# Optimization experiments

Measured on AMD Instinct MI355X. Metric: run time of the kernel, lower is better.

Reference implementation:

```python
import jax, jax.numpy as jnp
import numpy as np

B, N = 2, 512
CS, CZ, C, H, PQK, PV = 256, 128, 128, 8, 8, 12
INF, EPS = 1e5, 1e-8
ROPE_BASE = 10000.0


def _rotate_half(x):
    x1, x2 = jnp.split(x, 2, axis=-1)
    return jnp.concatenate([-x2, x1], axis=-1)


def _rope_cos_sin(n, dim):
    inv_freq = 1.0 / (ROPE_BASE ** (jnp.arange(0, dim, 2, dtype=jnp.float32) / dim))
    freqs = jnp.outer(jnp.arange(n, dtype=jnp.float32), inv_freq)
    emb = jnp.concatenate([freqs, freqs], axis=-1)  # [n, dim]
    return jnp.cos(emb), jnp.sin(emb)


def setup_inputs():
    key = jax.random.key(0)
    ks = jax.random.split(key, 16)
    s = jax.random.normal(ks[0], (B, N, CS), jnp.float32)
    z = jax.random.normal(ks[1], (B, N, N, CZ), jnp.float32)
    # random rigid frames: rotations from unit quaternions, translations ~ protein scale
    q4 = jax.random.normal(ks[2], (B, N, 4), jnp.float32)
    q4 = q4 / jnp.linalg.norm(q4, axis=-1, keepdims=True)
    w, x, y, zz = q4[..., 0], q4[..., 1], q4[..., 2], q4[..., 3]
    rot = jnp.stack([
        1 - 2 * (y * y + zz * zz), 2 * (x * y - w * zz), 2 * (x * zz + w * y),
        2 * (x * y + w * zz), 1 - 2 * (x * x + zz * zz), 2 * (y * zz - w * x),
        2 * (x * zz - w * y), 2 * (y * zz + w * x), 1 - 2 * (x * x + y * y)],
        axis=-1).reshape(B, N, 3, 3)
    trans = jax.random.normal(ks[3], (B, N, 3), jnp.float32) * 10.0
    mask = jnp.ones((B, N), jnp.float32)

    def nrm(k, shape, sc=0.02):
        return jax.random.normal(k, shape, jnp.float32) * sc

    HC = H * C
    params = dict(
        wq=nrm(ks[4], (HC, CS)), bq=jnp.zeros((HC,), jnp.float32),
        wkv=nrm(ks[5], (2 * HC, CS)), bkv=jnp.zeros((2 * HC,), jnp.float32),
        wqp=nrm(ks[6], (H * PQK * 3, CS)), bqp=jnp.zeros((H * PQK * 3,), jnp.float32),
        wkvp=nrm(ks[7], (H * (PQK + PV) * 3, CS)), bkvp=jnp.zeros((H * (PQK + PV) * 3,), jnp.float32),
        wb=nrm(ks[8], (H, CZ)), bb=jnp.zeros((H,), jnp.float32),
        head_weights=jnp.full((H,), 0.541324854612918, jnp.float32),  # softplus^-1(1)
        wout=nrm(ks[9], (CS, H * CZ + HC + H * PV * 4)), bout=jnp.zeros((CS,), jnp.float32),
    )
    return dict(s=s, z=z, rot=rot, trans=trans, mask=mask, **params)


def _ipa(s, z, rot, trans, mask, wq, bq, wkv, bkv, wqp, bqp, wkvp, bkvp, wb, bb,
         head_weights, wout, bout):
    # scalar q/k/v
    q = (s @ wq.T + bq).reshape(B, N, H, C)
    kv = (s @ wkv.T + bkv).reshape(B, N, H, 2 * C)
    k, v = jnp.split(kv, 2, axis=-1)
    # rotary embedding on scalar q/k (dim = c_hidden, positions = arange(N))
    cos, sin = _rope_cos_sin(N, C)
    cos = cos[None, :, None, :]
    sin = sin[None, :, None, :]
    q = q * cos + _rotate_half(q) * sin
    k = k * cos + _rotate_half(k) * sin
    # query/key/value points, mapped into the global frame (OpenFold split-then-stack layout)
    qp = s @ wqp.T + bqp
    qp = jnp.stack(jnp.split(qp, 3, axis=-1), axis=-1)  # [B,N,H*PQK,3]
    qp = jnp.einsum('bnij,bnpj->bnpi', rot, qp) + trans[:, :, None, :]
    q_pts = qp.reshape(B, N, H, PQK, 3)
    kvp = s @ wkvp.T + bkvp
    kvp = jnp.stack(jnp.split(kvp, 3, axis=-1), axis=-1)  # [B,N,H*(PQK+PV),3]
    kvp = jnp.einsum('bnij,bnpj->bnpi', rot, kvp) + trans[:, :, None, :]
    kvp = kvp.reshape(B, N, H, PQK + PV, 3)
    k_pts, v_pts = kvp[..., :PQK, :], kvp[..., PQK:, :]
    # pair bias
    bias = z @ wb.T + bb  # [B,N,N,H]
    # scalar attention logits
    a = jnp.einsum('bihc,bjhc->bhij', q, k) * np.float32(np.sqrt(1.0 / (3 * C)))
    a = a + np.float32(np.sqrt(1.0 / 3)) * jnp.transpose(bias, (0, 3, 1, 2))
    # point-distance attention
    disp = q_pts[:, :, None] - k_pts[:, None]           # [B,N,N,H,PQK,3]
    pt_att = jnp.sum(disp * disp, axis=-1)              # [B,N,N,H,PQK]
    hw = jax.nn.softplus(head_weights) * np.float32(np.sqrt(1.0 / (3 * (PQK * 9.0 / 2))))
    pt_att = -0.5 * jnp.sum(pt_att * hw[None, None, None, :, None], axis=-1)  # [B,N,N,H]
    sq_mask = (mask[:, :, None] * mask[:, None, :] - 1.0) * INF
    a = a + jnp.transpose(pt_att, (0, 3, 1, 2)) + sq_mask[:, None]
    a = jax.nn.softmax(a, axis=-1)  # [B,H,N,N]
    # outputs: scalar, points (inverse frame), point norms, pair
    o = jnp.einsum('bhij,bjhc->bihc', a, v).reshape(B, N, H * C)
    o_pt = jnp.einsum('bhij,bjhpx->bihpx', a, v_pts)    # [B,N,H,PV,3]
    o_pt = jnp.einsum('bnji,bnhpj->bnhpi', rot, o_pt - trans[:, :, None, None, :])
    o_pt_norm = jnp.sqrt(jnp.sum(o_pt * o_pt, axis=-1) + EPS).reshape(B, N, H * PV)
    o_pt_flat = jnp.moveaxis(o_pt, -1, 2).reshape(B, N, 3 * H * PV)  # x-block,y-block,z-block
    o_pair = jnp.einsum('bhij,bijc->bihc', a, z).reshape(B, N, H * CZ)
    feats = jnp.concatenate([o, o_pt_flat, o_pt_norm, o_pair], axis=-1)
    return feats @ wout.T + bout  # [B,N,CS]


def reference(s, z, rot, trans, mask, wq, bq, wkv, bkv, wqp, bqp, wkvp, bkvp, wb, bb,
              head_weights, wout, bout):
    return _ipa(s, z, rot, trans, mask, wq, bq, wkv, bkv, wqp, bqp, wkvp, bkvp,
                wb, bb, head_weights, wout, bout)
```

## Files before the change

kernel.cpp:

```cpp
#include <hip/hip_runtime.h>
#include <cstdint>


#define NROWS 3744
#define FEATS 2432

constexpr size_t OFF_RAW  = 0;
constexpr size_t OFF_Q    = 3833856;
constexpr size_t OFF_K    = OFF_Q + 1048576;
constexpr size_t OFF_V    = OFF_K + 1048576;
constexpr size_t OFF_QP   = OFF_V + 1048576;
constexpr size_t OFF_KP   = OFF_QP + 196608;
constexpr size_t OFF_VP   = OFF_KP + 196608;
constexpr size_t OFF_BIAS = OFF_VP + 294912;
constexpr size_t OFF_LG   = OFF_BIAS + 4194304;
constexpr size_t OFF_PART = OFF_LG + 4194304;

__device__ __forceinline__ void fma4(float4& acc, float s, const float4& v) {
    acc.x += s * v.x; acc.y += s * v.y; acc.z += s * v.z; acc.w += s * v.w;
}
__device__ __forceinline__ float dot4(const float4& a, const float4& b) {
    return a.x*b.x + a.y*b.y + a.z*b.z + a.w*b.w;
}

__global__ __launch_bounds__(256) void proj_gemm(
    const float* __restrict__ s,
    const float* __restrict__ wq,  const float* __restrict__ bq,
    const float* __restrict__ wkv, const float* __restrict__ bkv,
    const float* __restrict__ wqp, const float* __restrict__ bqp,
    const float* __restrict__ wkvp,const float* __restrict__ bkvp,
    float* __restrict__ raw)
{
    const int tile = blockIdx.x & 15;
    const int grp  = blockIdx.x >> 4;
    const int bn0  = tile * 64;
    const int r0   = grp * 128;
    __shared__ float s_lds[64 * 33];
    __shared__ float w_lds[128 * 33];
    const int t  = threadIdx.x;
    const int rg = t & 31;
    const int tg = t >> 5;

    float acc[4][8];
#pragma unroll
    for (int q = 0; q < 4; ++q)
#pragma unroll
        for (int w = 0; w < 8; ++w) acc[q][w] = 0.f;

    for (int kt = 0; kt < 8; ++kt) {
        const int fb = kt * 32;
        __syncthreads();
        for (int idx = t; idx < 64 * 32; idx += 256) {
            int il = idx >> 5, f = idx & 31;
            s_lds[il * 33 + f] = s[(size_t)(bn0 + il) * 256 + fb + f];
        }
        for (int idx = t; idx < 128 * 32; idx += 256) {
            int r = idx >> 5, f = idx & 31;
            int row = r0 + r;
            int ff = fb + f;
            float wv = 0.f;
            if (row < 1024)       wv = wq  [(size_t)row * 256 + ff];
            else if (row < 3072)  wv = wkv [(size_t)(row - 1024) * 256 + ff];
            else if (row < 3264)  wv = wqp [(size_t)(row - 3072) * 256 + ff];
            else if (row < 3744)  wv = wkvp[(size_t)(row - 3264) * 256 + ff];
            w_lds[r * 33 + f] = wv;
        }
        __syncthreads();
#pragma unroll
        for (int f = 0; f < 32; ++f) {
            float wv[4], sv[8];
#pragma unroll
            for (int q = 0; q < 4; ++q) wv[q] = w_lds[(rg + 32 * q) * 33 + f];
#pragma unroll
            for (int w = 0; w < 8; ++w) sv[w] = s_lds[(tg * 8 + w) * 33 + f];
#pragma unroll
            for (int q = 0; q < 4; ++q)
#pragma unroll
                for (int w = 0; w < 8; ++w) acc[q][w] += wv[q] * sv[w];
        }
    }
#pragma unroll
    for (int q = 0; q < 4; ++q) {
        int row = r0 + rg + 32 * q;
        if (row >= NROWS) continue;
        float bv;
        if (row < 1024)      bv = bq  [row];
        else if (row < 3072) bv = bkv [row - 1024];
        else if (row < 3264) bv = bqp [row - 3072];
        else                 bv = bkvp[row - 3264];
#pragma unroll
        for (int w = 0; w < 8; ++w)
            raw[(size_t)(bn0 + tg * 8 + w) * NROWS + row] = acc[q][w] + bv;
    }
}

__global__ __launch_bounds__(256) void post_k(
    const float* __restrict__ raw, const float* __restrict__ rot,
    const float* __restrict__ trans,
    float* __restrict__ q, float* __restrict__ k, float* __restrict__ v,
    float* __restrict__ qp, float* __restrict__ kp, float* __restrict__ vp)
{
    const int bn = blockIdx.x;
    const int b = bn >> 9, n = bn & 511;
    const int t = threadIdx.x;
    __shared__ float r_lds[NROWS];
    for (int idx = t; idx < NROWS; idx += 256)
        r_lds[idx] = raw[(size_t)bn * NROWS + idx];
    __syncthreads();

    const float LOG_BASE = 9.210340371976184f;

    for (int idx = t; idx < 1024; idx += 256) {
        int h = idx >> 7, c = idx & 127;
        int d = c & 63;
        float inv = expf(-(2.f * d / 128.f) * LOG_BASE);
        float sn, cs; sincosf((float)n * inv, &sn, &cs);
        float val = r_lds[idx];
        float pt  = (c < 64) ? -r_lds[idx + 64] : r_lds[idx - 64];
        q[(((size_t)(b * 8 + h)) * 512 + n) * 128 + c] = val * cs + pt * sn;
    }
    for (int idx = t; idx < 2048; idx += 256) {
        int h = idx >> 8, w = idx & 255;
        float val = r_lds[1024 + idx];
        if (w < 128) {
            int c = w, d = c & 63;
            float inv = expf(-(2.f * d / 128.f) * LOG_BASE);
            float sn, cs; sincosf((float)n * inv, &sn, &cs);
            float pt = (c < 64) ? -r_lds[1024 + h * 256 + c + 64]
                                :  r_lds[1024 + h * 256 + c - 64];
            k[(((size_t)(b * 8 + h)) * 512 + n) * 128 + c] = val * cs + pt * sn;
        } else {
            v[(((size_t)(b * 8 + h)) * 512 + n) * 128 + (w - 128)] = val;
        }
    }
    float R[9], T[3];
#pragma unroll
    for (int u = 0; u < 9; ++u) R[u] = rot[(size_t)bn * 9 + u];
#pragma unroll
    for (int u = 0; u < 3; ++u) T[u] = trans[(size_t)bn * 3 + u];

    if (t < 64) {
        int p = t;
        float x0 = r_lds[3072 + p], x1 = r_lds[3072 + 64 + p], x2 = r_lds[3072 + 128 + p];
        int h = p >> 3, pq = p & 7;
        size_t base = (((size_t)(b * 8 + h)) * 512 + n) * 24 + pq * 3;
        qp[base + 0] = R[0]*x0 + R[1]*x1 + R[2]*x2 + T[0];
        qp[base + 1] = R[3]*x0 + R[4]*x1 + R[5]*x2 + T[1];
        qp[base + 2] = R[6]*x0 + R[7]*x1 + R[8]*x2 + T[2];
    }
    if (t < 160) {
        int p = t;
        float x0 = r_lds[3264 + p], x1 = r_lds[3264 + 160 + p], x2 = r_lds[3264 + 320 + p];
        float g0 = R[0]*x0 + R[1]*x1 + R[2]*x2 + T[0];
        float g1 = R[3]*x0 + R[4]*x1 + R[5]*x2 + T[1];
        float g2 = R[6]*x0 + R[7]*x1 + R[8]*x2 + T[2];
        int h = p / 20, pp = p % 20;
        if (pp < 8) {
            size_t base = (((size_t)(b * 8 + h)) * 512 + n) * 24 + pp * 3;
            kp[base + 0] = g0; kp[base + 1] = g1; kp[base + 2] = g2;
        } else {
            size_t base = (((size_t)(b * 8 + h)) * 512 + n) * 36 + (pp - 8) * 3;
            vp[base + 0] = g0; vp[base + 1] = g1; vp[base + 2] = g2;
        }
    }
}

__global__ __launch_bounds__(256) void bias_k(
    const float* __restrict__ z, const float* __restrict__ wb,
    const float* __restrict__ bb, float* __restrict__ bias_t)
{
    const int bi = blockIdx.x;
    const int b = bi >> 9, i = bi & 511;
    const int t = threadIdx.x;
    const float4* z0 = (const float4*)(z + ((size_t)bi * 512 + t) * 128);
    const float4* z1 = (const float4*)(z + ((size_t)bi * 512 + t + 256) * 128);
    const float4* wb4 = (const float4*)wb;
    float acc0[8], acc1[8];
#pragma unroll
    for (int h = 0; h < 8; ++h) { acc0[h] = 0.f; acc1[h] = 0.f; }
#pragma unroll 4
    for (int c4 = 0; c4 < 32; ++c4) {
        float4 a4 = z0[c4];
        float4 b4 = z1[c4];
#pragma unroll
        for (int h = 0; h < 8; ++h) {
            float4 w4 = wb4[h * 32 + c4];
            acc0[h] += dot4(a4, w4);
            acc1[h] += dot4(b4, w4);
        }
    }
#pragma unroll
    for (int h = 0; h < 8; ++h) {
        float bv = bb[h];
        size_t base = (((size_t)(b * 8 + h)) * 512 + i) * 512;
        bias_t[base + t]       = acc0[h] + bv;
        bias_t[base + t + 256] = acc1[h] + bv;
    }
}

#define SCALE_QK 0.05103103630798287f
#define SCALE_B  0.5773502691896258f
#define HW_SCALE 0.09622504486493764f

__global__ __launch_bounds__(256) void logits_k(
    const float* __restrict__ q, const float* __restrict__ k,
    const float* __restrict__ qp, const float* __restrict__ kp,
    const float* __restrict__ mask, const float* __restrict__ hw_in,
    const float* __restrict__ bias_t, float* __restrict__ lg)
{
    const int blk = blockIdx.x;
    const int jt = blk & 7, it = (blk >> 3) & 15, bh = blk >> 7;
    const int b = bh >> 3, h = bh & 7;
    const int i0 = it * 32, j0 = jt * 64;
    const int t = threadIdx.x;
    const float hw = log1pf(expf(hw_in[h])) * HW_SCALE;

    __shared__ float qe[32 * 156];
    __shared__ float ke[64 * 156];
    __shared__ float Qs[32], Ks[64], Mi[32], Mj[64];

    for (int idx = t; idx < 32 * 128; idx += 256) {
        int il = idx >> 7, c = idx & 127;
        qe[il * 156 + c] = q[((size_t)bh * 512 + i0 + il) * 128 + c] * SCALE_QK;
    }
    for (int idx = t; idx < 32 * 24; idx += 256) {
        int il = idx / 24, e = idx % 24;
        qe[il * 156 + 128 + e] = qp[((size_t)bh * 512 + i0 + il) * 24 + e] * hw;
    }
    for (int idx = t; idx < 64 * 128; idx += 256) {
        int jl = idx >> 7, c = idx & 127;
        ke[jl * 156 + c] = k[((size_t)bh * 512 + j0 + jl) * 128 + c];
    }
    for (int idx = t; idx < 64 * 24; idx += 256) {
        int jl = idx / 24, e = idx % 24;
        ke[jl * 156 + 128 + e] = kp[((size_t)bh * 512 + j0 + jl) * 24 + e];
    }
    if (t < 32) {
        float sum = 0.f;
        for (int e = 0; e < 24; ++e) {
            float vv = qp[((size_t)bh * 512 + i0 + t) * 24 + e];
            sum += vv * vv;
        }
        Qs[t] = sum;
        Mi[t] = mask[b * 512 + i0 + t];
    }
    if (t >= 64 && t < 128) {
        int jl = t - 64;
        float sum = 0.f;
        for (int e = 0; e < 24; ++e) {
            float vv = kp[((size_t)bh * 512 + j0 + jl) * 24 + e];
            sum += vv * vv;
        }
        Ks[jl] = sum;
        Mj[jl] = mask[b * 512 + j0 + jl];
    }
    __syncthreads();

    const int tr = t >> 4, tc = t & 15;
    float acc[2][4] = {{0.f,0.f,0.f,0.f},{0.f,0.f,0.f,0.f}};
    const float4* qe4 = (const float4*)qe;
    const float4* ke4 = (const float4*)ke;
#pragma unroll 2
    for (int c4 = 0; c4 < 38; ++c4) {
        float4 qa = qe4[tr * 39 + c4];
        float4 qb = qe4[(tr + 16) * 39 + c4];
#pragma unroll
        for (int qq = 0; qq < 4; ++qq) {
            float4 kv = ke4[(tc + 16 * qq) * 39 + c4];
            acc[0][qq] += dot4(qa, kv);
            acc[1][qq] += dot4(qb, kv);
        }
    }
#pragma unroll
    for (int a2 = 0; a2 < 2; ++a2) {
        int il = tr + 16 * a2, i = i0 + il;
#pragma unroll
        for (int qq = 0; qq < 4; ++qq) {
            int jl = tc + 16 * qq, j = j0 + jl;
            float lv = acc[a2][qq] - 0.5f * hw * (Qs[il] + Ks[jl])
                     + SCALE_B * bias_t[((size_t)bh * 512 + i) * 512 + j]
                     + (Mi[il] * Mj[jl] - 1.f) * 100000.f;
            lg[((size_t)bh * 512 + i) * 512 + j] = lv;
        }
    }
}

__global__ __launch_bounds__(256) void av_k2(
    const float* __restrict__ lg, const float* __restrict__ v,
    const float* __restrict__ vp, const float* __restrict__ rot,
    const float* __restrict__ trans, float* __restrict__ feats)
{
    const int blk = blockIdx.x;
    const int it = blk & 31, bh = blk >> 5;
    const int b = bh >> 3, h = bh & 7;
    const int i0 = it * 16;
    const int t = threadIdx.x;
    const int jg = t >> 5, c4 = t & 31;

    __shared__ __align__(16) float a_lds[16 * 512];
    __shared__ __align__(16) float o_red[16 * 128];
    __shared__ __align__(16) float p_red[16 * 36];
    __shared__ float red[256];
    __shared__ float rmax[16], rinv[16];

    {
        const float4* a4 = (const float4*)(lg + ((size_t)bh * 512 + i0) * 512);
        float4* al4 = (float4*)a_lds;
        for (int idx = t; idx < 16 * 128; idx += 256)
            al4[idx] = a4[idx];
    }
    __syncthreads();

    {
        const int r = t >> 4, l = t & 15;
        float m = -1e30f;
        for (int u = 0; u < 32; ++u)
            m = fmaxf(m, a_lds[r * 512 + l + 16 * u]);
        red[t] = m;
        __syncthreads();
        if (t < 16) {
            float mm = red[t * 16];
            for (int u = 1; u < 16; ++u) mm = fmaxf(mm, red[t * 16 + u]);
            rmax[t] = mm;
        }
        __syncthreads();
        float rm = rmax[r];
        float sacc = 0.f;
        for (int u = 0; u < 32; ++u) {
            int idx = r * 512 + l + 16 * u;
            float e = __expf(a_lds[idx] - rm);
            a_lds[idx] = e;
            sacc += e;
        }
        red[t] = sacc;
        __syncthreads();
        if (t < 16) {
            float ss = red[t * 16];
            for (int u = 1; u < 16; ++u) ss += red[t * 16 + u];
            rinv[t] = 1.f / ss;
        }
        __syncthreads();
    }

    const int jbase = jg * 64;
    float4 acc[16];

#pragma unroll
    for (int il = 0; il < 16; ++il) acc[il] = {0.f, 0.f, 0.f, 0.f};
    {
        const float4* v4 = (const float4*)(v + (size_t)bh * 512 * 128);
#pragma unroll 2
        for (int jj = 0; jj < 64; jj += 2) {
            int j = jbase + jj;
            float4 v0 = v4[(size_t)j * 32 + c4];
            float4 v1 = v4[(size_t)(j + 1) * 32 + c4];
#pragma unroll
            for (int il = 0; il < 16; ++il) {
                float2 av = *(const float2*)&a_lds[il * 512 + j];
                fma4(acc[il], av.x, v0);
                fma4(acc[il], av.y, v1);
            }
        }
    }
    __syncthreads();
#pragma unroll
    for (int r = 0; r < 8; ++r) {
        if (jg == r) {
#pragma unroll
            for (int il = 0; il < 16; ++il) {
                float4* d = (float4*)&o_red[il * 128 + c4 * 4];
                if (r == 0) *d = acc[il];
                else {
                    float4 cu = *d;
                    cu.x += acc[il].x; cu.y += acc[il].y;
                    cu.z += acc[il].z; cu.w += acc[il].w;
                    *d = cu;
                }
            }
        }
        __syncthreads();
    }

#pragma unroll
    for (int il = 0; il < 16; ++il) acc[il] = {0.f, 0.f, 0.f, 0.f};
    if (c4 < 9) {
        const float4* vp4 = (const float4*)(vp + (size_t)bh * 512 * 36);
#pragma unroll 2
        for (int jj = 0; jj < 64; jj += 2) {
            int j = jbase + jj;
            float4 p0 = vp4[(size_t)j * 9 + c4];
            float4 p1 = vp4[(size_t)(j + 1) * 9 + c4];
#pragma unroll
            for (int il = 0; il < 16; ++il) {
                float2 av = *(const float2*)&a_lds[il * 512 + j];
                fma4(acc[il], av.x, p0);
                fma4(acc[il], av.y, p1);
            }
        }
    }
    __syncthreads();
#pragma unroll
    for (int r = 0; r < 8; ++r) {
        if (jg == r && c4 < 9) {
#pragma unroll
            for (int il = 0; il < 16; ++il) {
                float4* d = (float4*)&p_red[il * 36 + c4 * 4];
                if (r == 0) *d = acc[il];
                else {
                    float4 cu = *d;
                    cu.x += acc[il].x; cu.y += acc[il].y;
                    cu.z += acc[il].z; cu.w += acc[il].w;
                    *d = cu;
                }
            }
        }
        __syncthreads();
    }

    for (int idx = t; idx < 16 * 32; idx += 256) {
        int il = idx >> 5;
        float4 val = ((float4*)o_red)[idx];
        float sc = rinv[il];
        val.x *= sc; val.y *= sc; val.z *= sc; val.w *= sc;
        ((float4*)(feats + (size_t)(b * 512 + i0 + il) * FEATS + h * 128))[idx & 31] = val;
    }
    if (t < 192) {
        int il2 = t / 12, p = t % 12;
        float sc = rinv[il2];
        int bn = b * 512 + i0 + il2;
        float R[9];
#pragma unroll
        for (int u = 0; u < 9; ++u) R[u] = rot[(size_t)bn * 9 + u];
        float T0 = trans[(size_t)bn * 3 + 0];
        float T1 = trans[(size_t)bn * 3 + 1];
        float T2 = trans[(size_t)bn * 3 + 2];
        float x  = p_red[il2 * 36 + p * 3 + 0] * sc - T0;
        float y  = p_red[il2 * 36 + p * 3 + 1] * sc - T1;
        float zz = p_red[il2 * 36 + p * 3 + 2] * sc - T2;
        float l0 = R[0] * x + R[3] * y + R[6] * zz;
        float l1 = R[1] * x + R[4] * y + R[7] * zz;
        float l2 = R[2] * x + R[5] * y + R[8] * zz;
        size_t base = (size_t)bn * FEATS;
        feats[base + 1024 +       h * 12 + p] = l0;
        feats[base + 1024 +  96 + h * 12 + p] = l1;
        feats[base + 1024 + 192 + h * 12 + p] = l2;
        feats[base + 1312 +       h * 12 + p] = sqrtf(l0*l0 + l1*l1 + l2*l2 + 1e-8f);
    }
}

__global__ __launch_bounds__(256) void opair_k2(
    const float* __restrict__ lg, const float* __restrict__ z,
    float* __restrict__ feats)
{
    const int bi = blockIdx.x;
    const int b = bi >> 9, i = bi & 511;
    const int t = threadIdx.x;
    const int jg = t >> 5, c4 = t & 31;

    __shared__ __align__(16) float a_lds[8 * 512];
    __shared__ __align__(16) float o_red[8 * 128];
    __shared__ float red[256];
    __shared__ float rmax[8], rinv[8];

    for (int idx = t; idx < 8 * 128; idx += 256) {
        int h = idx >> 7, jc = idx & 127;
        ((float4*)a_lds)[idx] =
            ((const float4*)(lg + (((size_t)(b * 8 + h)) * 512 + i) * 512))[jc];
    }
    __syncthreads();

    {
        const int r = t >> 5, l = t & 31;
        float m = -1e30f;
        for (int u = 0; u < 16; ++u)
            m = fmaxf(m, a_lds[r * 512 + l + 32 * u]);
        red[t] = m;
        __syncthreads();
        if (t < 8) {
            float mm = red[t * 32];
            for (int u = 1; u < 32; ++u) mm = fmaxf(mm, red[t * 32 + u]);
            rmax[t] = mm;
        }
        __syncthreads();
        float rm = rmax[r];
        float sacc = 0.f;
        for (int u = 0; u < 16; ++u) {
            int idx = r * 512 + l + 32 * u;
            float e = __expf(a_lds[idx] - rm);
            a_lds[idx] = e;
            sacc += e;
        }
        red[t] = sacc;
        __syncthreads();
        if (t < 8) {
            float ss = red[t * 32];
            for (int u = 1; u < 32; ++u) ss += red[t * 32 + u];
            rinv[t] = 1.f / ss;
        }
        __syncthreads();
    }

    const float4* z4 = (const float4*)(z + (size_t)bi * 512 * 128);
    float4 acc[8];
#pragma unroll
    for (int h = 0; h < 8; ++h) acc[h] = {0.f, 0.f, 0.f, 0.f};
    const int jbase = jg * 64;
#pragma unroll 2
    for (int jj = 0; jj < 64; jj += 2) {
        int j = jbase + jj;
        float4 z0 = z4[(size_t)j * 32 + c4];
        float4 z1 = z4[(size_t)(j + 1) * 32 + c4];
#pragma unroll
        for (int h = 0; h < 8; ++h) {
            float2 av = *(const float2*)&a_lds[h * 512 + j];
            fma4(acc[h], av.x, z0);
            fma4(acc[h], av.y, z1);
        }
    }
    __syncthreads();
#pragma unroll
    for (int r = 0; r < 8; ++r) {
        if (jg == r) {
#pragma unroll
            for (int h = 0; h < 8; ++h) {
                float4* d = (float4*)&o_red[h * 128 + c4 * 4];
                if (r == 0) *d = acc[h];
                else {
                    float4 cu = *d;
                    cu.x += acc[h].x; cu.y += acc[h].y;
                    cu.z += acc[h].z; cu.w += acc[h].w;
                    *d = cu;
                }
            }
        }
        __syncthreads();
    }
    {
        int h = t >> 5;
        float4 val = ((float4*)o_red)[t];
        float sc = rinv[h];
        val.x *= sc; val.y *= sc; val.z *= sc; val.w *= sc;
        ((float4*)(feats + (size_t)bi * FEATS + 1408))[t] = val;
    }
}

__global__ __launch_bounds__(256) void out_gemm(
    const float* __restrict__ feats, const float* __restrict__ wout,
    float* __restrict__ part)
{
    const int blk = blockIdx.x;
    const int ks = blk & 7, mg = (blk >> 3) & 1, tile = blk >> 4;
    const int bn0 = tile * 64, m0 = mg * 128, f0 = ks * 304;
    __shared__ float a_lds[64 * 17];
    __shared__ float w_lds[128 * 17];
    const int t = threadIdx.x;
    const int rg = t & 31, tg = t >> 5;
    float acc[4][8];
#pragma unroll
    for (int q = 0; q < 4; ++q)
#pragma unroll
        for (int w = 0; w < 8; ++w) acc[q][w] = 0.f;

    for (int kt = 0; kt < 19; ++kt) {
        const int fb = f0 + kt * 16;
        __syncthreads();
        for (int idx = t; idx < 64 * 16; idx += 256) {
            int il = idx >> 4, f = idx & 15;
            a_lds[il * 17 + f] = feats[(size_t)(bn0 + il) * FEATS + fb + f];
        }
        for (int idx = t; idx < 128 * 16; idx += 256) {
            int r = idx >> 4, f = idx & 15;
            w_lds[r * 17 + f] = wout[(size_t)(m0 + r) * FEATS + fb + f];
        }
        __syncthreads();
#pragma unroll
        for (int f = 0; f < 16; ++f) {
            float wv[4], sv[8];
#pragma unroll
            for (int q = 0; q < 4; ++q) wv[q] = w_lds[(rg + 32 * q) * 17 + f];
#pragma unroll
            for (int w = 0; w < 8; ++w) sv[w] = a_lds[(tg * 8 + w) * 17 + f];
#pragma unroll
            for (int q = 0; q < 4; ++q)
#pragma unroll
                for (int w = 0; w < 8; ++w) acc[q][w] += wv[q] * sv[w];
        }
    }
#pragma unroll
    for (int q = 0; q < 4; ++q)
#pragma unroll
        for (int w = 0; w < 8; ++w)
            part[(size_t)ks * 262144 + (size_t)(bn0 + tg * 8 + w) * 256 + m0 + rg + 32 * q]
                = acc[q][w];
}

__global__ __launch_bounds__(256) void out_reduce(
    const float* __restrict__ part, const float* __restrict__ bout,
    float* __restrict__ out)
{
    const int idx = blockIdx.x * 256 + threadIdx.x;
    const float4* b4 = (const float4*)bout;
    const float4* p4 = (const float4*)part;
    float4 s = b4[idx & 63];
#pragma unroll
    for (int ksplit = 0; ksplit < 8; ++ksplit) {
        float4 pv = p4[(size_t)ksplit * 65536 + idx];
        s.x += pv.x; s.y += pv.y; s.z += pv.z; s.w += pv.w;
    }
    ((float4*)out)[idx] = s;
}

extern "C" void kernel_launch(void* const* d_in, const int* in_sizes, int n_in,
                              void* d_out, int out_size, void* d_ws, size_t ws_size,
                              hipStream_t stream)
{
    (void)in_sizes; (void)n_in; (void)out_size; (void)ws_size;
    const float* s     = (const float*)d_in[0];
    const float* z     = (const float*)d_in[1];
    const float* rot   = (const float*)d_in[2];
    const float* trans = (const float*)d_in[3];
    const float* mask  = (const float*)d_in[4];
    const float* wq    = (const float*)d_in[5];
    const float* bq    = (const float*)d_in[6];
    const float* wkv   = (const float*)d_in[7];
    const float* bkv   = (const float*)d_in[8];
    const float* wqp   = (const float*)d_in[9];
    const float* bqp   = (const float*)d_in[10];
    const float* wkvp  = (const float*)d_in[11];
    const float* bkvp  = (const float*)d_in[12];
    const float* wb    = (const float*)d_in[13];
    const float* bb    = (const float*)d_in[14];
    const float* hw    = (const float*)d_in[15];
    const float* wout  = (const float*)d_in[16];
    const float* bout  = (const float*)d_in[17];

    float* ws    = (float*)d_ws;
    float* raw   = ws + OFF_RAW;
    float* qb    = ws + OFF_Q;
    float* kb    = ws + OFF_K;
    float* vb    = ws + OFF_V;
    float* qpb   = ws + OFF_QP;
    float* kpb   = ws + OFF_KP;
    float* vpb   = ws + OFF_VP;
    float* biasb = ws + OFF_BIAS;
    float* lgb   = ws + OFF_LG;
    float* partb = ws + OFF_PART;
    float* featsb = ws + OFF_RAW;

    proj_gemm<<<dim3(480), dim3(256), 0, stream>>>(s, wq, bq, wkv, bkv, wqp, bqp, wkvp, bkvp, raw);
    post_k<<<dim3(1024), dim3(256), 0, stream>>>(raw, rot, trans, qb, kb, vb, qpb, kpb, vpb);
    bias_k<<<dim3(1024), dim3(256), 0, stream>>>(z, wb, bb, biasb);
    logits_k<<<dim3(2048), dim3(256), 0, stream>>>(qb, kb, qpb, kpb, mask, hw, biasb, lgb);
    av_k2<<<dim3(512), dim3(256), 0, stream>>>(lgb, vb, vpb, rot, trans, featsb);
    opair_k2<<<dim3(1024), dim3(256), 0, stream>>>(lgb, z, featsb);
    out_gemm<<<dim3(256), dim3(256), 0, stream>>>(featsb, wout, partb);
    out_reduce<<<dim3(256), dim3(256), 0, stream>>>(partb, bout, (float*)d_out);
}
```

Before: 741.0 us.

## Vectorize GEMM tile loads, precompute RoPE tables, split bias kernel blocks

The projection and output GEMMs now load tiles into LDS as float4 with a padded stride and read float4 operands in the inner loop. The aim is fewer global and LDS instructions, though the new strides may bring back bank conflicts. post_k computes the 64 RoPE cos/sin values once per block into shared memory instead of running expf/sincosf per element. bias_k handles one j-half per block with twice as many blocks, which lowers register pressure and adds parallelism.

```diff
diff --git a/kernel.cpp b/kernel.cpp
--- a/kernel.cpp
+++ b/kernel.cpp
@@ -35,8 +35,8 @@
     const int grp  = blockIdx.x >> 4;
     const int bn0  = tile * 64;
     const int r0   = grp * 128;
-    __shared__ float s_lds[64 * 33];
-    __shared__ float w_lds[128 * 33];
+    __shared__ __align__(16) float s_lds[64 * 36];
+    __shared__ __align__(16) float w_lds[128 * 36];
     const int t  = threadIdx.x;
     const int rg = t & 31;
     const int tg = t >> 5;
@@ -50,33 +50,35 @@
     for (int kt = 0; kt < 8; ++kt) {
         const int fb = kt * 32;
         __syncthreads();
-        for (int idx = t; idx < 64 * 32; idx += 256) {
-            int il = idx >> 5, f = idx & 31;
-            s_lds[il * 33 + f] = s[(size_t)(bn0 + il) * 256 + fb + f];
-        }
-        for (int idx = t; idx < 128 * 32; idx += 256) {
-            int r = idx >> 5, f = idx & 31;
+        for (int idx = t; idx < 64 * 8; idx += 256) {
+            int il = idx >> 3, f4i = idx & 7;
+            ((float4*)(s_lds + il * 36))[f4i] =
+                ((const float4*)(s + (size_t)(bn0 + il) * 256 + fb))[f4i];
+        }
+        for (int idx = t; idx < 128 * 8; idx += 256) {
+            int r = idx >> 3, f4i = idx & 7;
             int row = r0 + r;
-            int ff = fb + f;
-            float wv = 0.f;
-            if (row < 1024)       wv = wq  [(size_t)row * 256 + ff];
-            else if (row < 3072)  wv = wkv [(size_t)(row - 1024) * 256 + ff];
-            else if (row < 3264)  wv = wqp [(size_t)(row - 3072) * 256 + ff];
-            else if (row < 3744)  wv = wkvp[(size_t)(row - 3264) * 256 + ff];
-            w_lds[r * 33 + f] = wv;
-        }
-        __syncthreads();
-#pragma unroll
-        for (int f = 0; f < 32; ++f) {
-            float wv[4], sv[8];
-#pragma unroll
-            for (int q = 0; q < 4; ++q) wv[q] = w_lds[(rg + 32 * q) * 33 + f];
-#pragma unroll
-            for (int w = 0; w < 8; ++w) sv[w] = s_lds[(tg * 8 + w) * 33 + f];
+            float4 wv = {0.f, 0.f, 0.f, 0.f};
+            if (row < 1024)       wv = ((const float4*)(wq   + (size_t)row * 256 + fb))[f4i];
+            else if (row < 3072)  wv = ((const float4*)(wkv  + (size_t)(row - 1024) * 256 + fb))[f4i];
+            else if (row < 3264)  wv = ((const float4*)(wqp  + (size_t)(row - 3072) * 256 + fb))[f4i];
+            else if (row < 3744)  wv = ((const float4*)(wkvp + (size_t)(row - 3264) * 256 + fb))[f4i];
+            ((float4*)(w_lds + r * 36))[f4i] = wv;
+        }
+        __syncthreads();
+        const float4* w4p = (const float4*)w_lds;
+        const float4* s4p = (const float4*)s_lds;
+#pragma unroll
+        for (int f4i = 0; f4i < 8; ++f4i) {
+            float4 wv[4], sv[8];
+#pragma unroll
+            for (int q = 0; q < 4; ++q) wv[q] = w4p[(rg + 32 * q) * 9 + f4i];
+#pragma unroll
+            for (int w = 0; w < 8; ++w) sv[w] = s4p[(tg * 8 + w) * 9 + f4i];
 #pragma unroll
             for (int q = 0; q < 4; ++q)
 #pragma unroll
-                for (int w = 0; w < 8; ++w) acc[q][w] += wv[q] * sv[w];
+                for (int w = 0; w < 8; ++w) acc[q][w] += dot4(wv[q], sv[w]);
         }
     }
 #pragma unroll
@@ -104,31 +106,32 @@
     const int b = bn >> 9, n = bn & 511;
     const int t = threadIdx.x;
     __shared__ float r_lds[NROWS];
+    __shared__ float ct[64], st[64];
     for (int idx = t; idx < NROWS; idx += 256)
         r_lds[idx] = raw[(size_t)bn * NROWS + idx];
+    if (t < 64) {
+        const float LOG_BASE = 9.210340371976184f;
+        float inv = expf(-((float)t / 64.f) * LOG_BASE);
+        float sn, cs; sincosf((float)n * inv, &sn, &cs);
+        ct[t] = cs; st[t] = sn;
+    }
     __syncthreads();
 
-    const float LOG_BASE = 9.210340371976184f;
-
     for (int idx = t; idx < 1024; idx += 256) {
-        int h = idx >> 7, c = idx & 127;
-        int d = c & 63;
-        float inv = expf(-(2.f * d / 128.f) * LOG_BASE);
-        float sn, cs; sincosf((float)n * inv, &sn, &cs);
+        int c = idx & 127, d = c & 63;
         float val = r_lds[idx];
         float pt  = (c < 64) ? -r_lds[idx + 64] : r_lds[idx - 64];
-        q[(((size_t)(b * 8 + h)) * 512 + n) * 128 + c] = val * cs + pt * sn;
+        int h = idx >> 7;
+        q[(((size_t)(b * 8 + h)) * 512 + n) * 128 + c] = val * ct[d] + pt * st[d];
     }
     for (int idx = t; idx < 2048; idx += 256) {
         int h = idx >> 8, w = idx & 255;
         float val = r_lds[1024 + idx];
         if (w < 128) {
             int c = w, d = c & 63;
-            float inv = expf(-(2.f * d / 128.f) * LOG_BASE);
-            float sn, cs; sincosf((float)n * inv, &sn, &cs);
             float pt = (c < 64) ? -r_lds[1024 + h * 256 + c + 64]
                                 :  r_lds[1024 + h * 256 + c - 64];
-            k[(((size_t)(b * 8 + h)) * 512 + n) * 128 + c] = val * cs + pt * sn;
+            k[(((size_t)(b * 8 + h)) * 512 + n) * 128 + c] = val * ct[d] + pt * st[d];
         } else {
             v[(((size_t)(b * 8 + h)) * 512 + n) * 128 + (w - 128)] = val;
         }
@@ -169,32 +172,28 @@
     const float* __restrict__ z, const float* __restrict__ wb,
     const float* __restrict__ bb, float* __restrict__ bias_t)
 {
-    const int bi = blockIdx.x;
+    const int blk = blockIdx.x;
+    const int half = blk & 1;
+    const int bi = blk >> 1;
     const int b = bi >> 9, i = bi & 511;
     const int t = threadIdx.x;
-    const float4* z0 = (const float4*)(z + ((size_t)bi * 512 + t) * 128);
-    const float4* z1 = (const float4*)(z + ((size_t)bi * 512 + t + 256) * 128);
+    const int j = half * 256 + t;
+    const float4* z0 = (const float4*)(z + ((size_t)bi * 512 + j) * 128);
     const float4* wb4 = (const float4*)wb;
-    float acc0[8], acc1[8];
-#pragma unroll
-    for (int h = 0; h < 8; ++h) { acc0[h] = 0.f; acc1[h] = 0.f; }
-#pragma unroll 4
+    float acc0[8];
+#pragma unroll
+    for (int h = 0; h < 8; ++h) acc0[h] = 0.f;
+#pragma unroll 8
     for (int c4 = 0; c4 < 32; ++c4) {
         float4 a4 = z0[c4];
-        float4 b4 = z1[c4];
-#pragma unroll
-        for (int h = 0; h < 8; ++h) {
-            float4 w4 = wb4[h * 32 + c4];
-            acc0[h] += dot4(a4, w4);
-            acc1[h] += dot4(b4, w4);
-        }
+#pragma unroll
+        for (int h = 0; h < 8; ++h)
+            acc0[h] += dot4(a4, wb4[h * 32 + c4]);
     }
 #pragma unroll
     for (int h = 0; h < 8; ++h) {
-        float bv = bb[h];
         size_t base = (((size_t)(b * 8 + h)) * 512 + i) * 512;
-        bias_t[base + t]       = acc0[h] + bv;
-        bias_t[base + t + 256] = acc1[h] + bv;
+        bias_t[base + j] = acc0[h] + bb[h];
     }
 }
 
@@ -551,8 +550,8 @@
     const int blk = blockIdx.x;
     const int ks = blk & 7, mg = (blk >> 3) & 1, tile = blk >> 4;
     const int bn0 = tile * 64, m0 = mg * 128, f0 = ks * 304;
-    __shared__ float a_lds[64 * 17];
-    __shared__ float w_lds[128 * 17];
+    __shared__ __align__(16) float a_lds[64 * 20];
+    __shared__ __align__(16) float w_lds[128 * 20];
     const int t = threadIdx.x;
     const int rg = t & 31, tg = t >> 5;
     float acc[4][8];
@@ -564,26 +563,30 @@
     for (int kt = 0; kt < 19; ++kt) {
         const int fb = f0 + kt * 16;
         __syncthreads();
-        for (int idx = t; idx < 64 * 16; idx += 256) {
-            int il = idx >> 4, f = idx & 15;
-            a_lds[il * 17 + f] = feats[(size_t)(bn0 + il) * FEATS + fb + f];
-        }
-        for (int idx = t; idx < 128 * 16; idx += 256) {
-            int r = idx >> 4, f = idx & 15;
-            w_lds[r * 17 + f] = wout[(size_t)(m0 + r) * FEATS + fb + f];
-        }
-        __syncthreads();
-#pragma unroll
-        for (int f = 0; f < 16; ++f) {
-            float wv[4], sv[8];
-#pragma unroll
-            for (int q = 0; q < 4; ++q) wv[q] = w_lds[(rg + 32 * q) * 17 + f];
-#pragma unroll
-            for (int w = 0; w < 8; ++w) sv[w] = a_lds[(tg * 8 + w) * 17 + f];
+        for (int idx = t; idx < 64 * 4; idx += 256) {
+            int il = idx >> 2, f4i = idx & 3;
+            ((float4*)(a_lds + il * 20))[f4i] =
+                ((const float4*)(feats + (size_t)(bn0 + il) * FEATS + fb))[f4i];
+        }
+        for (int idx = t; idx < 128 * 4; idx += 256) {
+            int r = idx >> 2, f4i = idx & 3;
+            ((float4*)(w_lds + r * 20))[f4i] =
+                ((const float4*)(wout + (size_t)(m0 + r) * FEATS + fb))[f4i];
+        }
+        __syncthreads();
+        const float4* w4p = (const float4*)w_lds;
+        const float4* a4p = (const float4*)a_lds;
+#pragma unroll
+        for (int f4i = 0; f4i < 4; ++f4i) {
+            float4 wv[4], sv[8];
+#pragma unroll
+            for (int q = 0; q < 4; ++q) wv[q] = w4p[(rg + 32 * q) * 5 + f4i];
+#pragma unroll
+            for (int w = 0; w < 8; ++w) sv[w] = a4p[(tg * 8 + w) * 5 + f4i];
 #pragma unroll
             for (int q = 0; q < 4; ++q)
 #pragma unroll
-                for (int w = 0; w < 8; ++w) acc[q][w] += wv[q] * sv[w];
+                for (int w = 0; w < 8; ++w) acc[q][w] += dot4(wv[q], sv[w]);
         }
     }
 #pragma unroll
@@ -649,7 +652,7 @@
 
     proj_gemm<<<dim3(480), dim3(256), 0, stream>>>(s, wq, bq, wkv, bkv, wqp, bqp, wkvp, bkvp, raw);
     post_k<<<dim3(1024), dim3(256), 0, stream>>>(raw, rot, trans, qb, kb, vb, qpb, kpb, vpb);
-    bias_k<<<dim3(1024), dim3(256), 0, stream>>>(z, wb, bb, biasb);
+    bias_k<<<dim3(2048), dim3(256), 0, stream>>>(z, wb, bb, biasb);
     logits_k<<<dim3(2048), dim3(256), 0, stream>>>(qb, kb, qpb, kpb, mask, hw, biasb, lgb);
     av_k2<<<dim3(512), dim3(256), 0, stream>>>(lgb, vb, vpb, rot, trans, featsb);
     opair_k2<<<dim3(1024), dim3(256), 0, stream>>>(lgb, z, featsb);
```

Measured after the change: 707.1 us. 1.05x faster.
